# Kernel optimization log

Hardware: AMD Instinct MI355X
Metric: run time of the kernel (lower is better)

Reference implementation:

```python
import jax, jax.numpy as jnp
import numpy as np
import math

B, L, E, H, D = 2, 2048, 2048, 16, 128
LOGIT_SCALE_MAX = math.log(1.0 / 0.01)
EPS = 1e-6


def rms_norm(x, scale, eps=EPS):
    # UIOLayerNorm: no mean subtraction, no bias, fp32 internals
    x32 = x.astype(jnp.float32)
    ms = jnp.mean(x32 * x32, axis=-1, keepdims=True)
    return (scale * (x32 * jax.lax.rsqrt(ms + eps)).astype(x.dtype)).astype(x.dtype)


def apply_rotary(x, rope):
    # x: [b, l, h, d]; rope: [b, l, d] interpreted as (cos, sin) interleaved pairs
    b, l, h, d = x.shape
    xr = x.astype(jnp.float32).reshape(b, l, h, d // 2, 2)
    rc = rope.astype(jnp.float32).reshape(b, l, 1, d // 2, 2)
    out = jnp.stack(
        [xr[..., 0] * rc[..., 0] - xr[..., 1] * rc[..., 1],
         xr[..., 1] * rc[..., 0] + xr[..., 0] * rc[..., 1]], axis=-1)
    return out.reshape(b, l, h, d).astype(x.dtype)


def l2_normalize(x, eps=1e-12):
    # matches F.normalize(dim=-1): x / max(||x||, eps)
    n = jnp.sqrt(jnp.sum(x * x, axis=-1, keepdims=True))
    return x / jnp.maximum(n, eps)


def setup_inputs() -> dict:
    key = jax.random.key(0)
    ks = jax.random.split(key, 12)
    scale = 1.0 / math.sqrt(E)
    return {
        "inputs_q": jax.random.normal(ks[0], (B, L, E), jnp.float32),
        "inputs_kv": jax.random.normal(ks[1], (B, L, E), jnp.float32),
        "bias": jax.random.normal(ks[2], (1, 1, L, L), jnp.float32),
        "q_sinusoids": jax.random.uniform(ks[3], (B, L, D), jnp.float32, -1.0, 1.0),
        "k_sinusoids": jax.random.uniform(ks[4], (B, L, D), jnp.float32, -1.0, 1.0),
        "Wq": jax.random.normal(ks[5], (E, E), jnp.float32) * scale,
        "Wk": jax.random.normal(ks[6], (E, E), jnp.float32) * scale,
        "Wv": jax.random.normal(ks[7], (E, E), jnp.float32) * scale,
        "Wo": jax.random.normal(ks[8], (E, E), jnp.float32) * scale,
        "q_norm_scale": jnp.ones((D,), jnp.float32),
        "k_norm_scale": jnp.ones((D,), jnp.float32),
        "logit_scale": jnp.full((H,), math.log(10.0), jnp.float32),
    }


def reference(inputs_q, inputs_kv, bias, q_sinusoids, k_sinusoids,
              Wq, Wk, Wv, Wo, q_norm_scale, k_norm_scale, logit_scale):
    dtype = inputs_q.dtype
    b, ql, e = inputs_q.shape
    kl = inputs_kv.shape[1]
    # QKV projections (nn.Linear, no bias), split heads -> [b, len, h, d]
    q = (inputs_q @ Wq.T).reshape(b, ql, H, D)
    k = (inputs_kv @ Wk.T).reshape(b, kl, H, D)
    v = (inputs_kv @ Wv.T).reshape(b, kl, H, D)
    # qk_norm (UIO RMS norm over head_dim)
    q = rms_norm(q, q_norm_scale)
    k = rms_norm(k, k_norm_scale)
    # RoPE
    q = apply_rotary(q, q_sinusoids)
    k = apply_rotary(k, k_sinusoids)
    # float32_logits
    q32 = q.astype(jnp.float32)
    k32 = k.astype(jnp.float32)
    # scaled cosine attention: L2-normalize q,k; learned per-head logit scale
    scores = jnp.einsum("bqhd,bkhd->bhqk", l2_normalize(q32), l2_normalize(k32))
    ls = jnp.exp(jnp.minimum(logit_scale, LOGIT_SCALE_MAX))
    scores = scores * ls[None, :, None, None]
    scores = scores + bias.astype(scores.dtype)
    attn = jax.nn.softmax(scores, axis=-1).astype(dtype)
    out = jnp.einsum("bhqk,bkhd->bqhd", attn, v)
    out = out.reshape(b, ql, e)
    return out @ Wo.T
```

## Files before the change

### kernel.cpp

```cpp
#include <hip/hip_runtime.h>
#include <hip/hip_bf16.h>

#define B_ 2
#define L_ 2048
#define E_ 2048
#define H_ 16
#define D_ 128
#define M_ (B_*L_)
#define LOGIT_SCALE_MAX_ 4.6051701859880914f
#define LOG2E_ 1.44269504088896f

typedef __bf16 bf16_t;
typedef __bf16 bf16x2 __attribute__((ext_vector_type(2)));
typedef __bf16 bf16x4 __attribute__((ext_vector_type(4)));
typedef __bf16 bf16x8 __attribute__((ext_vector_type(8)));
typedef float f32x4 __attribute__((ext_vector_type(4)));
typedef float f32x16 __attribute__((ext_vector_type(16)));

#define KSB(p, r, cb) ((p) * 32768 + (r) * 256 + ((cb) ^ (((r) & 7) << 4)))
#define VSB(p, r, cb) ((p) * 32768 + 16384 + (r) * 128 + ((cb) ^ (((r) & 7) << 4)))

#define NW_ 4194304L
#define NX_ 8388608L

__global__ void cvt_all_k(const float* __restrict__ xq, const float* __restrict__ xkv,
                          const float* __restrict__ bias,
                          const float* __restrict__ wq, const float* __restrict__ wk,
                          const float* __restrict__ wv, const float* __restrict__ wo,
                          bf16_t* __restrict__ ws) {
    const long NW4 = NW_ / 4, NX4 = NX_ / 4;
    long i4 = (long)blockIdx.x * 256 + threadIdx.x;
    const float* src; long off; float scale = 1.0f;
    if (i4 < 4 * NW4) {
        long r = i4 / NW4;
        src = (r == 0) ? wq : (r == 1) ? wk : (r == 2) ? wv : wo;
        off = i4 - r * NW4;
    } else if (i4 < 5 * NW4) {
        src = bias; off = i4 - 4 * NW4; scale = LOG2E_;
    } else if (i4 < 5 * NW4 + NX4) {
        src = xq; off = i4 - 5 * NW4;
    } else {
        src = xkv; off = i4 - 5 * NW4 - NX4;
    }
    float4 v = ((const float4*)src)[off];
    bf16x4 o = { (bf16_t)(v.x * scale), (bf16_t)(v.y * scale),
                 (bf16_t)(v.z * scale), (bf16_t)(v.w * scale) };
    ((bf16x4*)ws)[i4] = o;
}

template<typename OutT, int GROUPS, int FULLB>
__global__ __launch_bounds__(512, 2) void gemm_mix(
    const bf16_t* __restrict__ A0g, const bf16_t* __restrict__ A1g,
    const bf16_t* __restrict__ W0, OutT* __restrict__ C0) {
    __shared__ __align__(16) unsigned char smem[131072];
    const int tid = threadIdx.x;
    const int wid = tid >> 6, lane = tid & 63;
    const int fr = lane & 15, fq = lane >> 4;
    const int wm = wid >> 2, wn = wid & 3;
    int slot, hsel, isfull;
    {
        int bid = blockIdx.x;
        if (FULLB > 0 && bid < FULLB) {
            slot = (bid & 7) * (FULLB >> 3) + (bid >> 3);
            hsel = 0; isfull = 1;
        } else {
            const int n = (int)gridDim.x - FULLB;
            int sub = bid - FULLB;
            int s = (sub & 7) * (n >> 3) + (sub >> 3);
            slot = FULLB + (s >> 1); hsel = s & 1; isfull = 0;
        }
    }
    const int g = slot >> 7;
    const int r0 = slot & 127;
    const int bm = r0 >> 3, bn = r0 & 7;
    const long arow0 = (long)bm * 256 + (long)hsel * 128;
    const long brow0 = (long)bn * 256;
    const bf16_t* Ab = ((GROUPS > 1 && g > 0) ? A1g : A0g) + arow0 * E_;
    const bf16_t* Wb = W0 + (long)g * (long)E_ * E_ + brow0 * E_;
    const int srow = tid >> 2;
    const int sc16 = tid & 3;

    auto STG = [&](const bf16_t* base, unsigned matOff, int h, unsigned bufb, int kt) {
        #pragma unroll
        for (int kk = 0; kk < 2; ++kk) {
            int col = kk * 32 + ((sc16 ^ ((srow >> 1) & 3)) * 8);
            __builtin_amdgcn_global_load_lds(
                (const __attribute__((address_space(1))) void*)(base + (long)(h * 128 + srow) * E_ + kt + col),
                (__attribute__((address_space(3))) void*)(smem + bufb + matOff + h * 16384u + kk * 8192u + tid * 16), 16, 0, 0);
        }
    };
    auto LDA = [&](unsigned pb, int kk, int r) -> bf16x8 {
        int lr = r & 127;
        return *(const bf16x8*)(smem + pb + (unsigned)(r >> 7) * 16384u + kk * 8192u + lr * 64 + ((fq ^ ((lr >> 1) & 3)) << 4));
    };
    auto LDB = [&](unsigned pb, int kk, int ni) -> bf16x8 {
        int r = wn * 64 + ni * 16 + fr;
        int lr = r & 127;
        return *(const bf16x8*)(smem + pb + 32768u + (unsigned)(r >> 7) * 16384u + kk * 8192u + lr * 64 + ((fq ^ ((lr >> 1) & 3)) << 4));
    };

    if (FULLB > 0 && isfull) {
        f32x4 acc[8][4] = {};
        STG(Ab, 0u,     0, 0u, 0); STG(Ab, 0u,     1, 0u, 0);
        STG(Wb, 32768u, 0, 0u, 0); STG(Wb, 32768u, 1, 0u, 0);
        STG(Wb, 32768u, 0, 65536u, 64); STG(Wb, 32768u, 1, 65536u, 64);
        asm volatile("s_waitcnt vmcnt(4)" ::: "memory");
        __builtin_amdgcn_s_barrier();
        bf16x8 bq[2][4];
        #pragma unroll 2
        for (int t = 0; t < 32; ++t) {
            const unsigned pb = (unsigned)(t & 1) * 65536u;
            const unsigned sbA = 65536u - pb;
            const int ktA = ((t + 1) & 31) * 64;
            const int ktB = ((t + 2) & 31) * 64;
            bf16x8 a[2][2];
            #pragma unroll
            for (int kk = 0; kk < 2; ++kk) {
                a[kk][0] = LDA(pb, kk, wm * 128 + 0 * 16 + fr);
                a[kk][1] = LDA(pb, kk, wm * 128 + 1 * 16 + fr);
                #pragma unroll
                for (int ni = 0; ni < 4; ++ni) bq[kk][ni] = LDB(pb, kk, ni);
            }
            STG(Ab, 0u, 0, sbA, ktA);
            __builtin_amdgcn_s_barrier();
            asm volatile("s_waitcnt lgkmcnt(0)" ::: "memory");
            __builtin_amdgcn_sched_barrier(0);
            __builtin_amdgcn_s_setprio(1);
            #pragma unroll
            for (int kk = 0; kk < 2; ++kk)
                #pragma unroll
                for (int ni = 0; ni < 4; ++ni) {
                    acc[0][ni] = __builtin_amdgcn_mfma_f32_16x16x32_bf16(a[kk][0], bq[kk][ni], acc[0][ni], 0, 0, 0);
                    acc[1][ni] = __builtin_amdgcn_mfma_f32_16x16x32_bf16(a[kk][1], bq[kk][ni], acc[1][ni], 0, 0, 0);
                }
            __builtin_amdgcn_s_setprio(0);
            __builtin_amdgcn_s_barrier();
            #pragma unroll
            for (int kk = 0; kk < 2; ++kk) {
                a[kk][0] = LDA(pb, kk, wm * 128 + 2 * 16 + fr);
                a[kk][1] = LDA(pb, kk, wm * 128 + 3 * 16 + fr);
            }
            STG(Ab, 0u, 1, sbA, ktA);
            __builtin_amdgcn_s_barrier();
            asm volatile("s_waitcnt lgkmcnt(0)" ::: "memory");
            __builtin_amdgcn_sched_barrier(0);
            __builtin_amdgcn_s_setprio(1);
            #pragma unroll
            for (int kk = 0; kk < 2; ++kk)
                #pragma unroll
                for (int ni = 0; ni < 4; ++ni) {
                    acc[2][ni] = __builtin_amdgcn_mfma_f32_16x16x32_bf16(a[kk][0], bq[kk][ni], acc[2][ni], 0, 0, 0);
                    acc[3][ni] = __builtin_amdgcn_mfma_f32_16x16x32_bf16(a[kk][1], bq[kk][ni], acc[3][ni], 0, 0, 0);
                }
            __builtin_amdgcn_s_setprio(0);
            __builtin_amdgcn_s_barrier();
            #pragma unroll
            for (int kk = 0; kk < 2; ++kk) {
                a[kk][0] = LDA(pb, kk, wm * 128 + 4 * 16 + fr);
                a[kk][1] = LDA(pb, kk, wm * 128 + 5 * 16 + fr);
            }
            STG(Wb, 32768u, 0, pb, ktB);
            __builtin_amdgcn_s_barrier();
            asm volatile("s_waitcnt lgkmcnt(0)" ::: "memory");
            __builtin_amdgcn_sched_barrier(0);
            __builtin_amdgcn_s_setprio(1);
            #pragma unroll
            for (int kk = 0; kk < 2; ++kk)
                #pragma unroll
                for (int ni = 0; ni < 4; ++ni) {
                    acc[4][ni] = __builtin_amdgcn_mfma_f32_16x16x32_bf16(a[kk][0], bq[kk][ni], acc[4][ni], 0, 0, 0);
                    acc[5][ni] = __builtin_amdgcn_mfma_f32_16x16x32_bf16(a[kk][1], bq[kk][ni], acc[5][ni], 0, 0, 0);
                }
            __builtin_amdgcn_s_setprio(0);
            __builtin_amdgcn_s_barrier();
            #pragma unroll
            for (int kk = 0; kk < 2; ++kk) {
                a[kk][0] = LDA(pb, kk, wm * 128 + 6 * 16 + fr);
                a[kk][1] = LDA(pb, kk, wm * 128 + 7 * 16 + fr);
            }
            STG(Wb, 32768u, 1, pb, ktB);
            asm volatile("s_waitcnt vmcnt(4)" ::: "memory");
            __builtin_amdgcn_s_barrier();
            asm volatile("s_waitcnt lgkmcnt(0)" ::: "memory");
            __builtin_amdgcn_sched_barrier(0);
            __builtin_amdgcn_s_setprio(1);
            #pragma unroll
            for (int kk = 0; kk < 2; ++kk)
                #pragma unroll
                for (int ni = 0; ni < 4; ++ni) {
                    acc[6][ni] = __builtin_amdgcn_mfma_f32_16x16x32_bf16(a[kk][0], bq[kk][ni], acc[6][ni], 0, 0, 0);
                    acc[7][ni] = __builtin_amdgcn_mfma_f32_16x16x32_bf16(a[kk][1], bq[kk][ni], acc[7][ni], 0, 0, 0);
                }
            __builtin_amdgcn_s_setprio(0);
            __builtin_amdgcn_s_barrier();
        }
        asm volatile("s_waitcnt vmcnt(0)" ::: "memory");
        OutT* Cg = C0 + (long)g * M_ * E_;
        #pragma unroll
        for (int mi = 0; mi < 8; ++mi)
            #pragma unroll
            for (int i = 0; i < 4; ++i) {
                long row = arow0 + wm * 128 + mi * 16 + fq * 4 + i;
                OutT* crow = Cg + row * E_ + brow0 + wn * 64 + fr;
                #pragma unroll
                for (int ni = 0; ni < 4; ++ni)
                    crow[ni * 16] = (OutT)acc[mi][ni][i];
            }
    } else {
        f32x4 acc[4][4] = {};
        STG(Ab, 0u,     0, 0u, 0);
        STG(Wb, 32768u, 0, 0u, 0); STG(Wb, 32768u, 1, 0u, 0);
        STG(Wb, 32768u, 0, 65536u, 64); STG(Wb, 32768u, 1, 65536u, 64);
        asm volatile("s_waitcnt vmcnt(4)" ::: "memory");
        __builtin_amdgcn_s_barrier();
        bf16x8 bq[2][4];
        #pragma unroll 2
        for (int t = 0; t < 32; ++t) {
            const unsigned pb = (unsigned)(t & 1) * 65536u;
            const unsigned sbA = 65536u - pb;
            const int ktA = ((t + 1) & 31) * 64;
            const int ktB = ((t + 2) & 31) * 64;
            bf16x8 a[2];
            #pragma unroll
            for (int kk = 0; kk < 2; ++kk) {
                a[kk] = LDA(pb, kk, wm * 64 + 0 * 16 + fr);
                #pragma unroll
                for (int ni = 0; ni < 4; ++ni) bq[kk][ni] = LDB(pb, kk, ni);
            }
            STG(Ab, 0u, 0, sbA, ktA);
            __builtin_amdgcn_s_barrier();
            asm volatile("s_waitcnt lgkmcnt(0)" ::: "memory");
            __builtin_amdgcn_sched_barrier(0);
            __builtin_amdgcn_s_setprio(1);
            #pragma unroll
            for (int kk = 0; kk < 2; ++kk)
                #pragma unroll
                for (int ni = 0; ni < 4; ++ni)
                    acc[0][ni] = __builtin_amdgcn_mfma_f32_16x16x32_bf16(a[kk], bq[kk][ni], acc[0][ni], 0, 0, 0);
            __builtin_amdgcn_s_setprio(0);
            __builtin_amdgcn_s_barrier();
            #pragma unroll
            for (int kk = 0; kk < 2; ++kk) a[kk] = LDA(pb, kk, wm * 64 + 1 * 16 + fr);
            __builtin_amdgcn_s_barrier();
            asm volatile("s_waitcnt lgkmcnt(0)" ::: "memory");
            __builtin_amdgcn_sched_barrier(0);
            __builtin_amdgcn_s_setprio(1);
            #pragma unroll
            for (int kk = 0; kk < 2; ++kk)
                #pragma unroll
                for (int ni = 0; ni < 4; ++ni)
                    acc[1][ni] = __builtin_amdgcn_mfma_f32_16x16x32_bf16(a[kk], bq[kk][ni], acc[1][ni], 0, 0, 0);
            __builtin_amdgcn_s_setprio(0);
            __builtin_amdgcn_s_barrier();
            #pragma unroll
            for (int kk = 0; kk < 2; ++kk) a[kk] = LDA(pb, kk, wm * 64 + 2 * 16 + fr);
            STG(Wb, 32768u, 0, pb, ktB);
            __builtin_amdgcn_s_barrier();
            asm volatile("s_waitcnt lgkmcnt(0)" ::: "memory");
            __builtin_amdgcn_sched_barrier(0);
            __builtin_amdgcn_s_setprio(1);
            #pragma unroll
            for (int kk = 0; kk < 2; ++kk)
                #pragma unroll
                for (int ni = 0; ni < 4; ++ni)
                    acc[2][ni] = __builtin_amdgcn_mfma_f32_16x16x32_bf16(a[kk], bq[kk][ni], acc[2][ni], 0, 0, 0);
            __builtin_amdgcn_s_setprio(0);
            __builtin_amdgcn_s_barrier();
            #pragma unroll
            for (int kk = 0; kk < 2; ++kk) a[kk] = LDA(pb, kk, wm * 64 + 3 * 16 + fr);
            STG(Wb, 32768u, 1, pb, ktB);
            asm volatile("s_waitcnt vmcnt(4)" ::: "memory");
            __builtin_amdgcn_s_barrier();
            asm volatile("s_waitcnt lgkmcnt(0)" ::: "memory");
            __builtin_amdgcn_sched_barrier(0);
            __builtin_amdgcn_s_setprio(1);
            #pragma unroll
            for (int kk = 0; kk < 2; ++kk)
                #pragma unroll
                for (int ni = 0; ni < 4; ++ni)
                    acc[3][ni] = __builtin_amdgcn_mfma_f32_16x16x32_bf16(a[kk], bq[kk][ni], acc[3][ni], 0, 0, 0);
            __builtin_amdgcn_s_setprio(0);
            __builtin_amdgcn_s_barrier();
        }
        asm volatile("s_waitcnt vmcnt(0)" ::: "memory");
        OutT* Cg = C0 + (long)g * M_ * E_;
        #pragma unroll
        for (int mi = 0; mi < 4; ++mi)
            #pragma unroll
            for (int i = 0; i < 4; ++i) {
                long row = arow0 + wm * 64 + mi * 16 + fq * 4 + i;
                OutT* crow = Cg + row * E_ + brow0 + wn * 64 + fr;
                #pragma unroll
                for (int ni = 0; ni < 4; ++ni)
                    crow[ni * 16] = (OutT)acc[mi][ni][i];
            }
    }
}

__global__ __launch_bounds__(256) void post_tv_k(
    const bf16_t* __restrict__ Pq, const bf16_t* __restrict__ Pk,
    const bf16_t* __restrict__ Vp,
    const float* __restrict__ qsins, const float* __restrict__ ksins,
    const float* __restrict__ qnscale, const float* __restrict__ knscale,
    bf16_t* __restrict__ outq, bf16_t* __restrict__ outk, bf16_t* __restrict__ Vt) {
    __shared__ bf16_t t[64 * 64];
    if (blockIdx.x < 32768) {
        const int wid = threadIdx.x >> 6, lane = threadIdx.x & 63;
        const int half = blockIdx.x >> 14;
        const long g = (long)(blockIdx.x & 16383) * 4 + wid;
        const bf16_t* P = half ? Pk : Pq;
        const float* sins = half ? ksins : qsins;
        const float* nscale = half ? knscale : qnscale;
        bf16_t* out = half ? outk : outq;
        const int h = (int)(g % H_);
        const long bl = g / H_;
        const int b = (int)(bl / L_), l = (int)(bl % L_);
        bf16x2 xv = *(const bf16x2*)(P + g * D_ + lane * 2);
        float x0 = (float)xv[0], x1 = (float)xv[1];
        float ss = x0 * x0 + x1 * x1;
        #pragma unroll
        for (int m = 1; m < 64; m <<= 1) ss += __shfl_xor(ss, m);
        float r = rsqrtf(ss * (1.0f / 128.0f) + 1e-6f);
        float y0 = x0 * r * nscale[lane * 2];
        float y1 = x1 * r * nscale[lane * 2 + 1];
        float2 cs = *(const float2*)(sins + bl * D_ + lane * 2);
        float z0 = y0 * cs.x - y1 * cs.y;
        float z1 = y1 * cs.x + y0 * cs.y;
        float n2 = z0 * z0 + z1 * z1;
        #pragma unroll
        for (int m = 1; m < 64; m <<= 1) n2 += __shfl_xor(n2, m);
        float inv = 1.0f / fmaxf(sqrtf(n2), 1e-12f);
        bf16x2 o = { (bf16_t)(z0 * inv), (bf16_t)(z1 * inv) };
        *(bf16x2*)(out + (((long)b * H_ + h) * L_ + l) * D_ + lane * 2) = o;
    } else {
        const int idx = blockIdx.x - 32768;
        const int lb = idx & 31;
        const int db = (idx >> 5) & 1;
        const int bh = idx >> 6;
        const int b = bh >> 4, h = bh & 15;
        const bf16_t* src = Vp + ((long)(b * L_ + lb * 64) * H_ + h) * D_ + db * 64;
        #pragma unroll
        for (int it = 0; it < 2; ++it) {
            int i = it * 256 + threadIdx.x;
            int r = i >> 3, c8 = i & 7;
            bf16x8 v = *(const bf16x8*)(src + (long)r * H_ * D_ + c8 * 8);
            *(bf16x8*)&t[r * 64 + (c8 ^ (r >> 3)) * 8] = v;
        }
        __syncthreads();
        bf16_t* dst = Vt + ((long)(b * H_ + h) * D_ + db * 64) * L_ + lb * 64;
        #pragma unroll
        for (int it = 0; it < 2; ++it) {
            int i = it * 256 + threadIdx.x;
            int d = i >> 3, l8 = i & 7;
            bf16x8 o;
            #pragma unroll
            for (int j = 0; j < 8; ++j) {
                int l = l8 * 8 + j;
                o[j] = t[l * 64 + ((d >> 3) ^ l8) * 8 + (d & 7)];
            }
            *(bf16x8*)(dst + (long)d * L_ + l8 * 8) = o;
        }
    }
}

__global__ __launch_bounds__(256, 2) void attn_k(
    const bf16_t* __restrict__ Qn, const bf16_t* __restrict__ Kn,
    const bf16_t* __restrict__ Vt, const bf16_t* __restrict__ biasb,
    const float* __restrict__ lsg, bf16_t* __restrict__ AO) {
    __shared__ __align__(16) unsigned char smem[65536];
    const int tid = threadIdx.x;
    const int w = tid >> 6, lane = tid & 63;
    const int lane31 = lane & 31, hi = lane >> 5;
    const int qb = blockIdx.x, bh = blockIdx.y;
    const int b = bh >> 4, h = bh & 15;
    const float lsc2 = __expf(fminf(lsg[h], LOGIT_SCALE_MAX_)) * LOG2E_;
    const int qr0 = qb * 128;
    const int qloc = w * 32 + lane31;
    const bf16_t* qrow  = Qn + (((long)b * H_ + h) * L_ + qr0 + qloc) * D_;
    const bf16_t* kbase = Kn + (((long)b * H_ + h) * L_) * D_;
    const bf16_t* vtbase = Vt + ((long)(b * H_ + h) * D_) * L_;
    const bf16_t* brow  = biasb + (long)(qr0 + qloc) * L_;

    const int ksr = tid >> 4, ksc = (tid & 15) * 8;
    const int vsr = tid >> 3, vsc = (tid & 7) * 8;

    bf16x8 qreg[8];
    #pragma unroll
    for (int kk = 0; kk < 8; ++kk)
        qreg[kk] = *(const bf16x8*)(qrow + kk * 16 + 8 * hi);

    f32x16 oacc[4] = {};
    float l_ = 0.f;

    bf16x8 kreg[4], vreg[4];
    #pragma unroll
    for (int it = 0; it < 4; ++it) {
        kreg[it] = *(const bf16x8*)(kbase + (long)(it * 16 + ksr) * D_ + ksc);
        vreg[it] = *(const bf16x8*)(vtbase + (long)(it * 32 + vsr) * L_ + vsc);
    }
    #pragma unroll
    for (int it = 0; it < 4; ++it) {
        *(bf16x8*)(smem + KSB(0, it * 16 + ksr, ksc * 2)) = kreg[it];
        *(bf16x8*)(smem + VSB(0, it * 32 + vsr, vsc * 2)) = vreg[it];
    }
    int p = 0;

    for (int kt = 0; kt < L_; kt += 64) {
        __syncthreads();
        const int ktn = (kt + 64 < L_) ? kt + 64 : 0;
        #pragma unroll
        for (int it = 0; it < 4; ++it) {
            kreg[it] = *(const bf16x8*)(kbase + (long)(ktn + it * 16 + ksr) * D_ + ksc);
            vreg[it] = *(const bf16x8*)(vtbase + (long)(it * 32 + vsr) * L_ + ktn + vsc);
        }
        bf16x4 bb[2][4];
        #pragma unroll
        for (int f = 0; f < 2; ++f)
            #pragma unroll
            for (int rr = 0; rr < 4; ++rr)
                bb[f][rr] = *(const bf16x4*)(brow + kt + f * 32 + rr * 8 + 4 * hi);
        f32x16 sacc[2] = {};
        __builtin_amdgcn_s_setprio(1);
        #pragma unroll
        for (int kk = 0; kk < 8; ++kk) {
            bf16x8 ak0 = *(const bf16x8*)(smem + KSB(p, lane31,      kk * 32 + 16 * hi));
            bf16x8 ak1 = *(const bf16x8*)(smem + KSB(p, 32 + lane31, kk * 32 + 16 * hi));
            sacc[0] = __builtin_amdgcn_mfma_f32_32x32x16_bf16(ak0, qreg[kk], sacc[0], 0, 0, 0);
            sacc[1] = __builtin_amdgcn_mfma_f32_32x32x16_bf16(ak1, qreg[kk], sacc[1], 0, 0, 0);
        }
        __builtin_amdgcn_s_setprio(0);
        float ps = 0.f;
        unsigned int wv[2][4][2];
        #pragma unroll
        for (int f = 0; f < 2; ++f)
            #pragma unroll
            for (int rr = 0; rr < 4; ++rr)
                #pragma unroll
                for (int wi = 0; wi < 2; ++wi) {
                    float pa = __builtin_amdgcn_exp2f(sacc[f][rr * 4 + wi * 2]     * lsc2 + (float)bb[f][rr][wi * 2]);
                    float pc = __builtin_amdgcn_exp2f(sacc[f][rr * 4 + wi * 2 + 1] * lsc2 + (float)bb[f][rr][wi * 2 + 1]);
                    ps += pa + pc;
                    bf16x2 t = { (bf16_t)pa, (bf16_t)pc };
                    wv[f][rr][wi] = __builtin_bit_cast(unsigned int, t);
                }
        ps += __shfl_xor(ps, 32);
        l_ += ps;
        bf16x8 pb_[4];
        #pragma unroll
        for (int kk = 0; kk < 4; ++kk) {
            const int f = kk >> 1;
            const int a2 = (kk & 1) * 2;
            unsigned int A0 = wv[f][a2][0],     A1 = wv[f][a2][1];
            unsigned int B0 = wv[f][a2 + 1][0], B1 = wv[f][a2 + 1][1];
            unsigned int own0  = hi ? B0 : A0;
            unsigned int own1  = hi ? B1 : A1;
            unsigned int send0 = hi ? A0 : B0;
            unsigned int send1 = hi ? A1 : B1;
            unsigned int recv0 = __shfl_xor(send0, 32);
            unsigned int recv1 = __shfl_xor(send1, 32);
            uint4 uu;
            uu.x = hi ? recv0 : own0;
            uu.y = hi ? recv1 : own1;
            uu.z = hi ? own0  : recv0;
            uu.w = hi ? own1  : recv1;
            pb_[kk] = __builtin_bit_cast(bf16x8, uu);
        }
        __builtin_amdgcn_s_setprio(1);
        #pragma unroll
        for (int df = 0; df < 4; ++df)
            #pragma unroll
            for (int kk = 0; kk < 4; ++kk) {
                bf16x8 av = *(const bf16x8*)(smem + VSB(p, df * 32 + lane31, kk * 32 + 16 * hi));
                oacc[df] = __builtin_amdgcn_mfma_f32_32x32x16_bf16(av, pb_[kk], oacc[df], 0, 0, 0);
            }
        __builtin_amdgcn_s_setprio(0);
        if (kt + 64 < L_) {
            #pragma unroll
            for (int it = 0; it < 4; ++it) {
                *(bf16x8*)(smem + KSB(p ^ 1, it * 16 + ksr, ksc * 2)) = kreg[it];
                *(bf16x8*)(smem + VSB(p ^ 1, it * 32 + vsr, vsc * 2)) = vreg[it];
            }
        }
        p ^= 1;
    }
    __syncthreads();
    float inv = 1.0f / l_;
    #pragma unroll
    for (int df = 0; df < 4; ++df)
        #pragma unroll
        for (int rg = 0; rg < 16; ++rg) {
            int d = df * 32 + (rg & 3) + 8 * (rg >> 2) + 4 * hi;
            *(bf16_t*)(smem + qloc * 264 + d * 2) = (bf16_t)(oacc[df][rg] * inv);
        }
    __syncthreads();
    #pragma unroll
    for (int it = 0; it < 8; ++it) {
        int idx = it * 256 + tid;
        int row = idx >> 4, c = idx & 15;
        bf16x8 v = *(const bf16x8*)(smem + row * 264 + c * 16);
        *(bf16x8*)(AO + ((long)b * L_ + qr0 + row) * E_ + h * D_ + c * 8) = v;
    }
}

extern "C" void kernel_launch(void* const* d_in, const int* in_sizes, int n_in,
                              void* d_out, int out_size, void* d_ws, size_t ws_size,
                              hipStream_t stream) {
    const float* inputs_q  = (const float*)d_in[0];
    const float* inputs_kv = (const float*)d_in[1];
    const float* bias      = (const float*)d_in[2];
    const float* q_sin     = (const float*)d_in[3];
    const float* k_sin     = (const float*)d_in[4];
    const float* Wq        = (const float*)d_in[5];
    const float* Wk        = (const float*)d_in[6];
    const float* Wv        = (const float*)d_in[7];
    const float* Wo        = (const float*)d_in[8];
    const float* qns       = (const float*)d_in[9];
    const float* kns       = (const float*)d_in[10];
    const float* lsg       = (const float*)d_in[11];

    bf16_t* ws = (bf16_t*)d_ws;
    const long NW = NW_;
    const long NX = NX_;
    bf16_t* Wq_b   = ws;
    bf16_t* Wo_b   = ws + 3 * NW;
    bf16_t* bias_b = ws + 4 * NW;
    bf16_t* Xq     = bias_b + NW;
    bf16_t* Xkv    = Xq + NX;
    bf16_t* Qp     = Xkv + NX;
    bf16_t* Kp     = Qp + NX;
    bf16_t* Vp     = Kp + NX;
    bf16_t* Qn = Xq;
    bf16_t* Kn = Xkv;
    bf16_t* AO = Qp;
    bf16_t* Vtr = Kp;
    if (ws_size < (size_t)(5 * NW + 5 * NX) * 2) return;

    {
        long n4 = (5 * NW + 2 * NX) / 4;
        cvt_all_k<<<dim3((unsigned)(n4 / 256)), dim3(256), 0, stream>>>(
            inputs_q, inputs_kv, bias, Wq, Wk, Wv, Wo, ws);
    }

    gemm_mix<bf16_t, 3, 256><<<dim3(512), dim3(512), 0, stream>>>(Xq, Xkv, Wq_b, Qp);

    post_tv_k<<<dim3(34816), dim3(256), 0, stream>>>(
        Qp, Kp, Vp, q_sin, k_sin, qns, kns, Qn, Kn, Vtr);

    attn_k<<<dim3(L_ / 128, B_ * H_), dim3(256), 0, stream>>>(Qn, Kn, Vtr, bias_b, lsg, AO);

    gemm_mix<float, 1, 0><<<dim3(256), dim3(512), 0, stream>>>(AO, AO, Wo_b, (float*)d_out);
}
```

Before: 316.8 us.

## Double attention query tile per block and stage K/V directly into LDS

Each attention block now covers 256 query rows, with every wave handling two 32-row query groups. Each staged K/V tile is therefore reused across twice as many queries, halving global K/V traffic per query. K/V staging switches from a register round trip plus LDS stores to global_load_lds direct-to-LDS loads, with the XOR swizzle applied on the global address side. The costs are half as many blocks (one per CU under launch_bounds(256,1)), lower occupancy to hide latency, higher register pressure, and an epilogue that writes output in two passes.

```diff
diff --git a/kernel.cpp b/kernel.cpp
--- a/kernel.cpp
+++ b/kernel.cpp
@@ -363,7 +363,7 @@
     }
 }
 
-__global__ __launch_bounds__(256, 2) void attn_k(
+__global__ __launch_bounds__(256, 1) void attn_k(
     const bf16_t* __restrict__ Qn, const bf16_t* __restrict__ Kn,
     const bf16_t* __restrict__ Vt, const bf16_t* __restrict__ biasb,
     const float* __restrict__ lsg, bf16_t* __restrict__ AO) {
@@ -374,96 +374,109 @@
     const int qb = blockIdx.x, bh = blockIdx.y;
     const int b = bh >> 4, h = bh & 15;
     const float lsc2 = __expf(fminf(lsg[h], LOGIT_SCALE_MAX_)) * LOG2E_;
-    const int qr0 = qb * 128;
-    const int qloc = w * 32 + lane31;
-    const bf16_t* qrow  = Qn + (((long)b * H_ + h) * L_ + qr0 + qloc) * D_;
+    const int qr0 = qb * 256;
     const bf16_t* kbase = Kn + (((long)b * H_ + h) * L_) * D_;
     const bf16_t* vtbase = Vt + ((long)(b * H_ + h) * D_) * L_;
-    const bf16_t* brow  = biasb + (long)(qr0 + qloc) * L_;
-
-    const int ksr = tid >> 4, ksc = (tid & 15) * 8;
-    const int vsr = tid >> 3, vsc = (tid & 7) * 8;
-
-    bf16x8 qreg[8];
+
+    bf16x8 qreg[2][8];
+    const bf16_t* brow[2];
     #pragma unroll
-    for (int kk = 0; kk < 8; ++kk)
-        qreg[kk] = *(const bf16x8*)(qrow + kk * 16 + 8 * hi);
-
-    f32x16 oacc[4] = {};
-    float l_ = 0.f;
-
-    bf16x8 kreg[4], vreg[4];
-    #pragma unroll
-    for (int it = 0; it < 4; ++it) {
-        kreg[it] = *(const bf16x8*)(kbase + (long)(it * 16 + ksr) * D_ + ksc);
-        vreg[it] = *(const bf16x8*)(vtbase + (long)(it * 32 + vsr) * L_ + vsc);
-    }
-    #pragma unroll
-    for (int it = 0; it < 4; ++it) {
-        *(bf16x8*)(smem + KSB(0, it * 16 + ksr, ksc * 2)) = kreg[it];
-        *(bf16x8*)(smem + VSB(0, it * 32 + vsr, vsc * 2)) = vreg[it];
-    }
+    for (int q2 = 0; q2 < 2; ++q2) {
+        const long qrow = (long)qr0 + w * 64 + q2 * 32 + lane31;
+        const bf16_t* qp = Qn + (((long)b * H_ + h) * L_ + qrow) * D_;
+        #pragma unroll
+        for (int kk = 0; kk < 8; ++kk)
+            qreg[q2][kk] = *(const bf16x8*)(qp + kk * 16 + 8 * hi);
+        brow[q2] = biasb + qrow * L_;
+    }
+
+    f32x16 oacc[2][4] = {};
+    float lsum[2] = {0.f, 0.f};
+
+    auto STAGE = [&](int p, int kt) {
+        #pragma unroll
+        for (int it = 0; it < 4; ++it) {
+            int ci = it * 256 + tid;
+            int kr = ci >> 4, kc = ci & 15;
+            __builtin_amdgcn_global_load_lds(
+                (const __attribute__((address_space(1))) void*)(kbase + (long)(kt + kr) * D_ + ((kc ^ (kr & 7)) * 8)),
+                (__attribute__((address_space(3))) void*)(smem + p * 32768 + ci * 16), 16, 0, 0);
+        }
+        #pragma unroll
+        for (int it = 0; it < 4; ++it) {
+            int ci = it * 256 + tid;
+            int vr = ci >> 3, vc = ci & 7;
+            __builtin_amdgcn_global_load_lds(
+                (const __attribute__((address_space(1))) void*)(vtbase + (long)vr * L_ + kt + ((vc ^ (vr & 7)) * 8)),
+                (__attribute__((address_space(3))) void*)(smem + p * 32768 + 16384 + ci * 16), 16, 0, 0);
+        }
+    };
+
+    STAGE(0, 0);
+    asm volatile("s_waitcnt vmcnt(0)" ::: "memory");
+    __builtin_amdgcn_s_barrier();
     int p = 0;
 
     for (int kt = 0; kt < L_; kt += 64) {
-        __syncthreads();
-        const int ktn = (kt + 64 < L_) ? kt + 64 : 0;
-        #pragma unroll
-        for (int it = 0; it < 4; ++it) {
-            kreg[it] = *(const bf16x8*)(kbase + (long)(ktn + it * 16 + ksr) * D_ + ksc);
-            vreg[it] = *(const bf16x8*)(vtbase + (long)(it * 32 + vsr) * L_ + ktn + vsc);
-        }
-        bf16x4 bb[2][4];
-        #pragma unroll
-        for (int f = 0; f < 2; ++f)
-            #pragma unroll
-            for (int rr = 0; rr < 4; ++rr)
-                bb[f][rr] = *(const bf16x4*)(brow + kt + f * 32 + rr * 8 + 4 * hi);
-        f32x16 sacc[2] = {};
+        if (kt + 64 < L_) STAGE(p ^ 1, kt + 64);
+        bf16x4 bb[2][2][4];
+        #pragma unroll
+        for (int q2 = 0; q2 < 2; ++q2)
+            #pragma unroll
+            for (int f = 0; f < 2; ++f)
+                #pragma unroll
+                for (int rr = 0; rr < 4; ++rr)
+                    bb[q2][f][rr] = *(const bf16x4*)(brow[q2] + kt + f * 32 + rr * 8 + 4 * hi);
+        f32x16 sacc[2][2] = {};
         __builtin_amdgcn_s_setprio(1);
         #pragma unroll
         for (int kk = 0; kk < 8; ++kk) {
             bf16x8 ak0 = *(const bf16x8*)(smem + KSB(p, lane31,      kk * 32 + 16 * hi));
             bf16x8 ak1 = *(const bf16x8*)(smem + KSB(p, 32 + lane31, kk * 32 + 16 * hi));
-            sacc[0] = __builtin_amdgcn_mfma_f32_32x32x16_bf16(ak0, qreg[kk], sacc[0], 0, 0, 0);
-            sacc[1] = __builtin_amdgcn_mfma_f32_32x32x16_bf16(ak1, qreg[kk], sacc[1], 0, 0, 0);
+            sacc[0][0] = __builtin_amdgcn_mfma_f32_32x32x16_bf16(ak0, qreg[0][kk], sacc[0][0], 0, 0, 0);
+            sacc[0][1] = __builtin_amdgcn_mfma_f32_32x32x16_bf16(ak1, qreg[0][kk], sacc[0][1], 0, 0, 0);
+            sacc[1][0] = __builtin_amdgcn_mfma_f32_32x32x16_bf16(ak0, qreg[1][kk], sacc[1][0], 0, 0, 0);
+            sacc[1][1] = __builtin_amdgcn_mfma_f32_32x32x16_bf16(ak1, qreg[1][kk], sacc[1][1], 0, 0, 0);
         }
         __builtin_amdgcn_s_setprio(0);
-        float ps = 0.f;
-        unsigned int wv[2][4][2];
-        #pragma unroll
-        for (int f = 0; f < 2; ++f)
-            #pragma unroll
-            for (int rr = 0; rr < 4; ++rr)
-                #pragma unroll
-                for (int wi = 0; wi < 2; ++wi) {
-                    float pa = __builtin_amdgcn_exp2f(sacc[f][rr * 4 + wi * 2]     * lsc2 + (float)bb[f][rr][wi * 2]);
-                    float pc = __builtin_amdgcn_exp2f(sacc[f][rr * 4 + wi * 2 + 1] * lsc2 + (float)bb[f][rr][wi * 2 + 1]);
-                    ps += pa + pc;
-                    bf16x2 t = { (bf16_t)pa, (bf16_t)pc };
-                    wv[f][rr][wi] = __builtin_bit_cast(unsigned int, t);
-                }
-        ps += __shfl_xor(ps, 32);
-        l_ += ps;
-        bf16x8 pb_[4];
-        #pragma unroll
-        for (int kk = 0; kk < 4; ++kk) {
-            const int f = kk >> 1;
-            const int a2 = (kk & 1) * 2;
-            unsigned int A0 = wv[f][a2][0],     A1 = wv[f][a2][1];
-            unsigned int B0 = wv[f][a2 + 1][0], B1 = wv[f][a2 + 1][1];
-            unsigned int own0  = hi ? B0 : A0;
-            unsigned int own1  = hi ? B1 : A1;
-            unsigned int send0 = hi ? A0 : B0;
-            unsigned int send1 = hi ? A1 : B1;
-            unsigned int recv0 = __shfl_xor(send0, 32);
-            unsigned int recv1 = __shfl_xor(send1, 32);
-            uint4 uu;
-            uu.x = hi ? recv0 : own0;
-            uu.y = hi ? recv1 : own1;
-            uu.z = hi ? own0  : recv0;
-            uu.w = hi ? own1  : recv1;
-            pb_[kk] = __builtin_bit_cast(bf16x8, uu);
+        bf16x8 pb_[2][4];
+        #pragma unroll
+        for (int q2 = 0; q2 < 2; ++q2) {
+            float ps = 0.f;
+            unsigned int wv[2][4][2];
+            #pragma unroll
+            for (int f = 0; f < 2; ++f)
+                #pragma unroll
+                for (int rr = 0; rr < 4; ++rr)
+                    #pragma unroll
+                    for (int wi = 0; wi < 2; ++wi) {
+                        float pa = __builtin_amdgcn_exp2f(sacc[q2][f][rr * 4 + wi * 2]     * lsc2 + (float)bb[q2][f][rr][wi * 2]);
+                        float pc = __builtin_amdgcn_exp2f(sacc[q2][f][rr * 4 + wi * 2 + 1] * lsc2 + (float)bb[q2][f][rr][wi * 2 + 1]);
+                        ps += pa + pc;
+                        bf16x2 t2 = { (bf16_t)pa, (bf16_t)pc };
+                        wv[f][rr][wi] = __builtin_bit_cast(unsigned int, t2);
+                    }
+            ps += __shfl_xor(ps, 32);
+            lsum[q2] += ps;
+            #pragma unroll
+            for (int kk = 0; kk < 4; ++kk) {
+                const int f = kk >> 1;
+                const int a2 = (kk & 1) * 2;
+                unsigned int A0 = wv[f][a2][0],     A1 = wv[f][a2][1];
+                unsigned int B0 = wv[f][a2 + 1][0], B1 = wv[f][a2 + 1][1];
+                unsigned int own0  = hi ? B0 : A0;
+                unsigned int own1  = hi ? B1 : A1;
+                unsigned int send0 = hi ? A0 : B0;
+                unsigned int send1 = hi ? A1 : B1;
+                unsigned int recv0 = __shfl_xor(send0, 32);
+                unsigned int recv1 = __shfl_xor(send1, 32);
+                uint4 uu;
+                uu.x = hi ? recv0 : own0;
+                uu.y = hi ? recv1 : own1;
+                uu.z = hi ? own0  : recv0;
+                uu.w = hi ? own1  : recv1;
+                pb_[q2][kk] = __builtin_bit_cast(bf16x8, uu);
+            }
         }
         __builtin_amdgcn_s_setprio(1);
         #pragma unroll
@@ -471,34 +484,34 @@
             #pragma unroll
             for (int kk = 0; kk < 4; ++kk) {
                 bf16x8 av = *(const bf16x8*)(smem + VSB(p, df * 32 + lane31, kk * 32 + 16 * hi));
-                oacc[df] = __builtin_amdgcn_mfma_f32_32x32x16_bf16(av, pb_[kk], oacc[df], 0, 0, 0);
+                oacc[0][df] = __builtin_amdgcn_mfma_f32_32x32x16_bf16(av, pb_[0][kk], oacc[0][df], 0, 0, 0);
+                oacc[1][df] = __builtin_amdgcn_mfma_f32_32x32x16_bf16(av, pb_[1][kk], oacc[1][df], 0, 0, 0);
             }
         __builtin_amdgcn_s_setprio(0);
-        if (kt + 64 < L_) {
-            #pragma unroll
-            for (int it = 0; it < 4; ++it) {
-                *(bf16x8*)(smem + KSB(p ^ 1, it * 16 + ksr, ksc * 2)) = kreg[it];
-                *(bf16x8*)(smem + VSB(p ^ 1, it * 32 + vsr, vsc * 2)) = vreg[it];
-            }
-        }
+        asm volatile("s_waitcnt vmcnt(0)" ::: "memory");
+        __builtin_amdgcn_s_barrier();
         p ^= 1;
     }
-    __syncthreads();
-    float inv = 1.0f / l_;
     #pragma unroll
-    for (int df = 0; df < 4; ++df)
-        #pragma unroll
-        for (int rg = 0; rg < 16; ++rg) {
-            int d = df * 32 + (rg & 3) + 8 * (rg >> 2) + 4 * hi;
-            *(bf16_t*)(smem + qloc * 264 + d * 2) = (bf16_t)(oacc[df][rg] * inv);
-        }
-    __syncthreads();
-    #pragma unroll
-    for (int it = 0; it < 8; ++it) {
-        int idx = it * 256 + tid;
-        int row = idx >> 4, c = idx & 15;
-        bf16x8 v = *(const bf16x8*)(smem + row * 264 + c * 16);
-        *(bf16x8*)(AO + ((long)b * L_ + qr0 + row) * E_ + h * D_ + c * 8) = v;
+    for (int q2 = 0; q2 < 2; ++q2) {
+        float inv = 1.0f / lsum[q2];
+        #pragma unroll
+        for (int df = 0; df < 4; ++df)
+            #pragma unroll
+            for (int rg = 0; rg < 16; ++rg) {
+                int d = df * 32 + (rg & 3) + 8 * (rg >> 2) + 4 * hi;
+                *(bf16_t*)(smem + (w * 32 + lane31) * 264 + d * 2) = (bf16_t)(oacc[q2][df][rg] * inv);
+            }
+        __syncthreads();
+        #pragma unroll
+        for (int it = 0; it < 8; ++it) {
+            int idx = it * 256 + tid;
+            int row = idx >> 4, c = idx & 15;
+            bf16x8 v = *(const bf16x8*)(smem + row * 264 + c * 16);
+            long orow = (long)qr0 + (row >> 5) * 64 + q2 * 32 + (row & 31);
+            *(bf16x8*)(AO + ((long)b * L_ + orow) * E_ + h * D_ + c * 8) = v;
+        }
+        __syncthreads();
     }
 }
 
@@ -546,7 +559,7 @@
     post_tv_k<<<dim3(34816), dim3(256), 0, stream>>>(
         Qp, Kp, Vp, q_sin, k_sin, qns, kns, Qn, Kn, Vtr);
 
-    attn_k<<<dim3(L_ / 128, B_ * H_), dim3(256), 0, stream>>>(Qn, Kn, Vtr, bias_b, lsg, AO);
+    attn_k<<<dim3(L_ / 256, B_ * H_), dim3(256), 0, stream>>>(Qn, Kn, Vtr, bias_b, lsg, AO);
 
     gemm_mix<float, 1, 0><<<dim3(256), dim3(512), 0, stream>>>(AO, AO, Wo_b, (float*)d_out);
 }
```

Result: slower. 368.0 us (+16.2%).
